# Optimization experiments

Measured on AMD Instinct MI355X. Metric: run time of the kernel, lower is better.

The kernel has to match this reference:

```python
import jax, jax.numpy as jnp
import numpy as np

# Dimensions
B, S, H = 2, 1024, 1024          # batch, seq_len, hidden_size
I, N, R, K = 2048, 16, 64, 4     # mamba: intermediate, state_size, dt_rank, conv_kernel
NH, NKV, HD = 16, 4, 64          # attention heads, kv heads, head_dim
W_ATT, W_SSM = 512, 128          # dual sliding window sizes
IM = 2816                        # SwiGLU intermediate: 256*ceil(1024*4*2/3/256)
EPS = 1e-6
ROPE_THETA = 10000.0
NEG = -1e9


def rms(x, w):
    return x * jax.lax.rsqrt(jnp.mean(x * x, axis=-1, keepdims=True) + EPS) * w


def silu(x):
    return x * jax.nn.sigmoid(x)


def rotary(x):
    # x: [B, S, h, HD]
    pos = jnp.arange(S, dtype=jnp.float32)
    inv = 1.0 / (ROPE_THETA ** (jnp.arange(0, HD, 2, dtype=jnp.float32) / HD))
    f = pos[:, None] * inv                                   # [S, HD/2]
    cos = jnp.concatenate([jnp.cos(f), jnp.cos(f)], -1)[None, :, None, :]
    sin = jnp.concatenate([jnp.sin(f), jnp.sin(f)], -1)[None, :, None, :]
    x1, x2 = x[..., : HD // 2], x[..., HD // 2 :]
    return x * cos + jnp.concatenate([-x2, x1], -1) * sin


def setup_inputs() -> dict:
    key = jax.random.key(0)
    ks = jax.random.split(key, 16)
    g = lambda k, shape, s=0.02: jax.random.normal(k, shape, jnp.float32) * s
    A_log = jnp.log(jnp.arange(1, N + 1, dtype=jnp.float32))[None, :] * jnp.ones((I, 1), jnp.float32)
    return {
        "hidden_states": jax.random.normal(ks[0], (B, S, H), jnp.float32),
        "pre_norm_w": jnp.ones((H,), jnp.float32),
        "in_proj_w": g(ks[1], (2 * I, H)),
        "conv_w": g(ks[2], (I, K), 0.2),
        "conv_b": jnp.zeros((I,), jnp.float32),
        "x_proj_w": g(ks[3], (R + 2 * N, I)),
        "dt_proj_w": g(ks[4], (I, R), 0.1),
        "dt_proj_b": jnp.full((I,), -2.0, jnp.float32),
        "A_log": A_log,
        "D": jnp.ones((I,), jnp.float32),
        "out_proj_w": g(ks[5], (H, I)),
        "ssm_norm_w": jnp.ones((H,), jnp.float32),
        "q_w": g(ks[6], (NH * HD, H)),
        "k_w": g(ks[7], (NKV * HD, H)),
        "v_w": g(ks[8], (NKV * HD, H)),
        "o_w": g(ks[9], (H, NH * HD)),
        "mlp_norm_w": jnp.ones((H,), jnp.float32),
        "gate_w": g(ks[10], (2 * IM, H)),
        "down_w": g(ks[11], (H, IM)),
    }


def reference(hidden_states, pre_norm_w, in_proj_w, conv_w, conv_b, x_proj_w,
              dt_proj_w, dt_proj_b, A_log, D, out_proj_w, ssm_norm_w,
              q_w, k_w, v_w, o_w, mlp_norm_w, gate_w, down_w):
    residual = hidden_states
    hs = rms(hidden_states, pre_norm_w)

    # ---- Mamba mixer (selective scan) ----
    xz = hs @ in_proj_w.T                          # [B,S,2I]
    x, z = jnp.split(xz, 2, -1)
    x_pad = jnp.pad(x, ((0, 0), (K - 1, 0), (0, 0)))  # causal depthwise conv
    xc = sum(conv_w[:, k] * x_pad[:, k : k + S, :] for k in range(K)) + conv_b
    xs = silu(xc)                                  # [B,S,I]
    proj = xs @ x_proj_w.T                         # [B,S,R+2N]
    dt = jax.nn.softplus(proj[..., :R] @ dt_proj_w.T + dt_proj_b)  # [B,S,I]
    Bm, Cm = proj[..., R : R + N], proj[..., R + N :]              # [B,S,N]
    A = -jnp.exp(A_log)                            # [I,N]
    dA = jnp.exp(dt[..., None] * A)                # [B,S,I,N]
    dBx = dt[..., None] * Bm[:, :, None, :] * xs[..., None]        # [B,S,I,N]

    def step(h, t):
        dA_t, dBx_t, C_t = t
        h = h * dA_t + dBx_t                       # [B,I,N]
        return h, jnp.einsum('bin,bn->bi', h, C_t)

    _, ys = jax.lax.scan(step, jnp.zeros((B, I, N), xs.dtype),
                         (dA.swapaxes(0, 1), dBx.swapaxes(0, 1), Cm.swapaxes(0, 1)))
    y = ys.swapaxes(0, 1) + D * xs
    y = y * silu(z)
    ssm_out = y @ out_proj_w.T                     # [B,S,H]

    # ---- fused add-norm ----
    ssm_residual = ssm_out + residual
    ssm_states = rms(ssm_residual, ssm_norm_w)

    # ---- dual sliding-window attention (GQA) ----
    q = rotary((hs @ q_w.T).reshape(B, S, NH, HD))
    k_att = rotary((hs @ k_w.T).reshape(B, S, NKV, HD))
    v_att = (hs @ v_w.T).reshape(B, S, NKV, HD)
    k_ssm = rotary((ssm_states @ k_w.T).reshape(B, S, NKV, HD))
    v_ssm = (ssm_states @ v_w.T).reshape(B, S, NKV, HD)
    rep = NH // NKV
    expand = lambda t: jnp.repeat(t, rep, axis=2)
    scale = HD ** -0.5
    pi = jnp.arange(S)
    d = pi[:, None] - pi[None, :]
    mask_att = (d >= 0) & (d < W_ATT)
    mask_ssm = (d >= 0) & (d < W_SSM)
    s_att = jnp.where(mask_att, jnp.einsum('bqhd,bkhd->bhqk', q, expand(k_att)) * scale, NEG)
    s_ssm = jnp.where(mask_ssm, jnp.einsum('bqhd,bkhd->bhqk', q, expand(k_ssm)) * scale, NEG)
    p = jax.nn.softmax(jnp.concatenate([s_att, s_ssm], -1), axis=-1)  # joint softmax
    p_att, p_ssm = jnp.split(p, 2, -1)
    o = (jnp.einsum('bhqk,bkhd->bqhd', p_att, expand(v_att)) +
         jnp.einsum('bhqk,bkhd->bqhd', p_ssm, expand(v_ssm)))
    att_out = o.reshape(B, S, NH * HD) @ o_w.T

    # ---- fused add-norm + SwiGLU MLP ----
    mlp_residual = att_out + ssm_residual
    x2 = rms(mlp_residual, mlp_norm_w)
    gate, yv = jnp.split(x2 @ gate_w.T, 2, -1)
    out = (silu(gate) * yv) @ down_w.T
    return mlp_residual + out
```

## Files before the change

### kernel.cpp

```cpp
#include <hip/hip_runtime.h>
#include <hip/hip_bf16.h>

using bf16 = __hip_bfloat16;
typedef short sh8 __attribute__((ext_vector_type(8)));
typedef float f32x4 __attribute__((ext_vector_type(4)));

constexpr int B_ = 2, S_ = 1024, H_ = 1024;
constexpr int I_ = 2048, N_ = 16, R_ = 64, K_ = 4;
constexpr int NH_ = 16, NKV_ = 4, HD_ = 64;
constexpr int IM_ = 2816;
constexpr int M_ = B_ * S_;
constexpr float EPS_ = 1e-6f;
constexpr int NC_ = 64;
constexpr int CL_ = S_ / NC_;
constexpr int BI_ = B_ * I_;

__device__ __forceinline__ float bf2f(bf16 v) { return __bfloat162float(v); }
__device__ __forceinline__ unsigned short f2bfu(float f) {
  bf16 h = __float2bfloat16(f);
  return *reinterpret_cast<unsigned short*>(&h);
}

constexpr int WOFF[11] = {
    0,
    4194304,
    4194304 + 196608,
    4390912 + 131072,
    4521984 + 2097152,
    6619136 + 1048576,
    7667712 + 262144,
    7929856 + 262144,
    8192000 + 1048576,
    9240576 + 5767168,
    15007744 + 2883584};
struct WPtrs { const float* p[10]; };

__global__ __launch_bounds__(256) void weights_cvt(WPtrs wp, bf16* __restrict__ dst) {
  int idx4 = blockIdx.x * 256 + threadIdx.x;
  if (idx4 >= WOFF[10] / 4) return;
  int e = idx4 * 4;
  int seg = 0;
#pragma unroll
  for (int s = 1; s < 10; ++s)
    if (e >= WOFF[s]) seg = s;
  float4 v = *(const float4*)(wp.p[seg] + (e - WOFF[seg]));
  ushort4 u = {f2bfu(v.x), f2bfu(v.y), f2bfu(v.z), f2bfu(v.w)};
  *(ushort4*)(dst + e) = u;
}

__global__ __launch_bounds__(256) void rms_kernel(const float* __restrict__ src,
                                                  const float* __restrict__ w,
                                                  bf16* __restrict__ dst, int ncols) {
  int row = blockIdx.x;
  const float* s = src + (size_t)row * ncols;
  float ss = 0.f;
  for (int c = threadIdx.x; c < ncols; c += 256) {
    float v = s[c];
    ss += v * v;
  }
#pragma unroll
  for (int off = 32; off; off >>= 1) ss += __shfl_down(ss, off, 64);
  __shared__ float red[4];
  if ((threadIdx.x & 63) == 0) red[threadIdx.x >> 6] = ss;
  __syncthreads();
  float tot = red[0] + red[1] + red[2] + red[3];
  float sc = rsqrtf(tot / (float)ncols + EPS_);
  for (int c = threadIdx.x; c < ncols; c += 256) {
    dst[(size_t)row * ncols + c] = __float2bfloat16(s[c] * sc * w[c]);
  }
}

__global__ __launch_bounds__(256) void reduce_rms_kernel(const float* __restrict__ parts,
                                                         int np, size_t pstride,
                                                         const float* __restrict__ residual,
                                                         float* __restrict__ sum_out,
                                                         const float* __restrict__ w,
                                                         bf16* __restrict__ dst) {
  int row = blockIdx.x;
  float v[4];
  float ss = 0.f;
#pragma unroll
  for (int e = 0; e < 4; ++e) {
    int c = threadIdx.x + e * 256;
    size_t o = (size_t)row * 1024 + c;
    float s = residual[o];
    for (int p = 0; p < np; ++p) s += parts[(size_t)p * pstride + o];
    v[e] = s;
    sum_out[o] = s;
    ss += s * s;
  }
#pragma unroll
  for (int off = 32; off; off >>= 1) ss += __shfl_down(ss, off, 64);
  __shared__ float red[4];
  if ((threadIdx.x & 63) == 0) red[threadIdx.x >> 6] = ss;
  __syncthreads();
  float tot = red[0] + red[1] + red[2] + red[3];
  float sc = rsqrtf(tot / 1024.f + EPS_);
#pragma unroll
  for (int e = 0; e < 4; ++e) {
    int c = threadIdx.x + e * 256;
    dst[(size_t)row * 1024 + c] = __float2bfloat16(v[e] * sc * w[c]);
  }
}

__global__ __launch_bounds__(256) void reduce_add_kernel(const float* __restrict__ parts,
                                                         int np, size_t pstride,
                                                         const float* __restrict__ residual,
                                                         float* __restrict__ out, int n4) {
  int idx = blockIdx.x * 256 + threadIdx.x;
  if (idx >= n4) return;
  float4 s = ((const float4*)residual)[idx];
  for (int p = 0; p < np; ++p) {
    float4 v = ((const float4*)(parts + (size_t)p * pstride))[idx];
    s.x += v.x; s.y += v.y; s.z += v.z; s.w += v.w;
  }
  ((float4*)out)[idx] = s;
}

__global__ __launch_bounds__(256) void xproj_reduce_kernel(const float* __restrict__ parts,
                                                           int np, size_t pstride,
                                                           float* __restrict__ proj,
                                                           bf16* __restrict__ proj_b, int n4) {
  int idx = blockIdx.x * 256 + threadIdx.x;
  if (idx >= n4) return;
  float4 s = {0.f, 0.f, 0.f, 0.f};
  for (int p = 0; p < np; ++p) {
    float4 v = ((const float4*)(parts + (size_t)p * pstride))[idx];
    s.x += v.x; s.y += v.y; s.z += v.z; s.w += v.w;
  }
  ((float4*)proj)[idx] = s;
  ushort4 u = {f2bfu(s.x), f2bfu(s.y), f2bfu(s.z), f2bfu(s.w)};
  ((ushort4*)proj_b)[idx] = u;
}

template <int MODE>
__global__ __launch_bounds__(256) void mfma_gemm_ep(const bf16* __restrict__ A,
                                                    const bf16* __restrict__ W,
                                                    float* __restrict__ C,
                                                    bf16* __restrict__ Cb,
                                                    int Nn, int Kd, int lda, int kclen,
                                                    size_t pstride,
                                                    const float* __restrict__ biasf) {
  __shared__ bf16 Als[128 * 64];
  __shared__ bf16 Bls[128 * 64];
  const int tid = threadIdx.x;
  const int lane = tid & 63;
  const int wave = tid >> 6;
  const int m0 = blockIdx.y * 128;
  const int n0 = blockIdx.x * 128;
  const int wm = (wave >> 1) * 64;
  const int wn = (wave & 1) * 64;
  const int kbeg = blockIdx.z * kclen;
  const int kend = min(Kd, kbeg + kclen);

  f32x4 acc[4][4] = {};

  for (int k0 = kbeg; k0 < kend; k0 += 64) {
#pragma unroll
    for (int r = 0; r < 4; ++r) {
      int linear = (r * 256 + tid) * 8;
      int row = linear >> 6;
      int col = linear & 63;
      const bf16* gA = A + (size_t)(m0 + row) * lda + (k0 + col);
      __builtin_amdgcn_global_load_lds(
          (const __attribute__((address_space(1))) void*)gA,
          (__attribute__((address_space(3))) void*)&Als[linear], 16, 0, 0);
      int nrow = n0 + row;
      if (nrow < Nn) {
        const bf16* gB = W + (size_t)nrow * Kd + (k0 + col);
        __builtin_amdgcn_global_load_lds(
            (const __attribute__((address_space(1))) void*)gB,
            (__attribute__((address_space(3))) void*)&Bls[linear], 16, 0, 0);
      }
    }
    __syncthreads();
#pragma unroll
    for (int kc = 0; kc < 2; ++kc) {
      const int kb = kc * 32 + (lane >> 4) * 8;
      sh8 af[4], bv[4];
#pragma unroll
      for (int i = 0; i < 4; ++i)
        af[i] = *reinterpret_cast<const sh8*>(&Als[(wm + i * 16 + (lane & 15)) * 64 + kb]);
#pragma unroll
      for (int j = 0; j < 4; ++j)
        bv[j] = *reinterpret_cast<const sh8*>(&Bls[(wn + j * 16 + (lane & 15)) * 64 + kb]);
#pragma unroll
      for (int i = 0; i < 4; ++i)
#pragma unroll
        for (int j = 0; j < 4; ++j)
          acc[i][j] = __builtin_amdgcn_mfma_f32_16x16x32_bf16(af[i], bv[j], acc[i][j], 0, 0, 0);
    }
    __syncthreads();
  }
#pragma unroll
  for (int i = 0; i < 4; ++i) {
#pragma unroll
    for (int j = 0; j < 4; ++j) {
      int col = n0 + wn + j * 16 + (lane & 15);
      if (col < Nn) {
#pragma unroll
        for (int r = 0; r < 4; ++r) {
          int row = m0 + wm + i * 16 + (lane >> 4) * 4 + r;
          size_t o = (size_t)row * Nn + col;
          float v = acc[i][j][r];
          if constexpr (MODE == 5) {
            Cb[o] = __float2bfloat16(v);
          } else if constexpr (MODE == 7) {
            float x = v + biasf[col];
            Cb[o] = __float2bfloat16((x > 20.f) ? x : log1pf(__expf(x)));
          } else if constexpr (MODE == 9) {
            C[(size_t)blockIdx.z * pstride + o] = v;
          }
        }
      }
    }
  }
}

__global__ __launch_bounds__(256) void conv_silu_kernel(const bf16* __restrict__ xz_b,
                                                        const float* __restrict__ cw,
                                                        const float* __restrict__ cb,
                                                        bf16* __restrict__ xs_b,
                                                        bf16* __restrict__ zs_b) {
  int idx4 = blockIdx.x * 256 + threadIdx.x;
  if (idx4 >= M_ * I_ / 4) return;
  int i4 = (idx4 & (I_ / 4 - 1)) * 4;
  int row = idx4 >> 9;
  int t = row & (S_ - 1);
  float4 acc = *(const float4*)(cb + i4);
  float a[4] = {acc.x, acc.y, acc.z, acc.w};
#pragma unroll
  for (int k = 0; k < K_; ++k) {
    int tt = t + k - (K_ - 1);
    if (tt >= 0) {
      const bf16* xp = xz_b + (size_t)(row + k - (K_ - 1)) * (2 * I_) + i4;
#pragma unroll
      for (int e = 0; e < 4; ++e)
        a[e] += cw[(i4 + e) * K_ + k] * bf2f(xp[e]);
    }
  }
  ushort4 xo, zo;
  const bf16* zp = xz_b + (size_t)row * (2 * I_) + I_ + i4;
#pragma unroll
  for (int e = 0; e < 4; ++e) {
    float sg = 1.f / (1.f + __expf(-a[e]));
    ((unsigned short*)&xo)[e] = f2bfu(a[e] * sg);
    float z = bf2f(zp[e]);
    float zg = 1.f / (1.f + __expf(-z));
    ((unsigned short*)&zo)[e] = f2bfu(z * zg);
  }
  *(ushort4*)(xs_b + (size_t)row * I_ + i4) = xo;
  *(ushort4*)(zs_b + (size_t)row * I_ + i4) = zo;
}

__global__ __launch_bounds__(256) void scan1_kernel(const bf16* __restrict__ dt_b,
                                                    const bf16* __restrict__ xs_b,
                                                    const float* __restrict__ proj,
                                                    const float* __restrict__ A_log,
                                                    float* __restrict__ aprod,
                                                    float* __restrict__ hloc) {
  const int b = blockIdx.x >> 3;
  const int i = (blockIdx.x & 7) * 256 + threadIdx.x;
  const int c = blockIdx.y;
  float A[16];
#pragma unroll
  for (int n = 0; n < 16; ++n) A[n] = -__expf(A_log[i * 16 + n]);
  float h[16] = {}, ap[16];
#pragma unroll
  for (int n = 0; n < 16; ++n) ap[n] = 1.f;
  const int t0 = c * CL_;
  for (int t = 0; t < CL_; ++t) {
    int row = b * S_ + t0 + t;
    float d = bf2f(dt_b[(size_t)row * I_ + i]);
    float x = bf2f(xs_b[(size_t)row * I_ + i]);
    const float* prow = proj + (size_t)row * 96 + R_;
    float dx = d * x;
#pragma unroll
    for (int q = 0; q < 4; ++q) {
      float4 Bv = *(const float4*)(prow + q * 4);
      float bvals[4] = {Bv.x, Bv.y, Bv.z, Bv.w};
#pragma unroll
      for (int n = 0; n < 4; ++n) {
        int nn = q * 4 + n;
        float da = __expf(d * A[nn]);
        h[nn] = h[nn] * da + dx * bvals[n];
        ap[nn] *= da;
      }
    }
  }
  size_t o = ((size_t)c * BI_ + (b << 11) + i) * 16;
#pragma unroll
  for (int n = 0; n < 16; ++n) { aprod[o + n] = ap[n]; hloc[o + n] = h[n]; }
}

__global__ __launch_bounds__(256) void scan2_kernel(const float* __restrict__ aprod,
                                                    const float* __restrict__ hloc,
                                                    float* __restrict__ hstart) {
  int j = blockIdx.x * 256 + threadIdx.x;
  float h = 0.f;
  for (int c = 0; c < NC_; ++c) {
    size_t idx = (size_t)c * (BI_ * 16) + j;
    hstart[idx] = h;
    h = aprod[idx] * h + hloc[idx];
  }
}

__global__ __launch_bounds__(256) void scan3_kernel(const bf16* __restrict__ dt_b,
                                                    const bf16* __restrict__ xs_b,
                                                    const float* __restrict__ proj,
                                                    const float* __restrict__ A_log,
                                                    const float* __restrict__ hstart,
                                                    const bf16* __restrict__ zs_b,
                                                    const float* __restrict__ Dp,
                                                    bf16* __restrict__ ys_b) {
  const int b = blockIdx.x >> 3;
  const int i = (blockIdx.x & 7) * 256 + threadIdx.x;
  const int c = blockIdx.y;
  float A[16];
#pragma unroll
  for (int n = 0; n < 16; ++n) A[n] = -__expf(A_log[i * 16 + n]);
  float h[16];
  size_t hs0 = ((size_t)c * BI_ + (b << 11) + i) * 16;
#pragma unroll
  for (int n = 0; n < 16; ++n) h[n] = hstart[hs0 + n];
  float Dv = Dp[i];
  const int t0 = c * CL_;
  for (int t = 0; t < CL_; ++t) {
    int row = b * S_ + t0 + t;
    float d = bf2f(dt_b[(size_t)row * I_ + i]);
    float x = bf2f(xs_b[(size_t)row * I_ + i]);
    const float* prow = proj + (size_t)row * 96 + R_;
    float dx = d * x;
    float y = 0.f;
#pragma unroll
    for (int q = 0; q < 4; ++q) {
      float4 Bv = *(const float4*)(prow + q * 4);
      float4 Cv = *(const float4*)(prow + 16 + q * 4);
      float bvals[4] = {Bv.x, Bv.y, Bv.z, Bv.w};
      float cvals[4] = {Cv.x, Cv.y, Cv.z, Cv.w};
#pragma unroll
      for (int n = 0; n < 4; ++n) {
        int nn = q * 4 + n;
        float da = __expf(d * A[nn]);
        h[nn] = h[nn] * da + dx * bvals[n];
        y += h[nn] * cvals[n];
      }
    }
    float yv = y + Dv * x;
    float zs = bf2f(zs_b[(size_t)row * I_ + i]);
    ys_b[(size_t)row * I_ + i] = __float2bfloat16(yv * zs);
  }
}

__global__ __launch_bounds__(256) void rope_all_kernel(const float* __restrict__ pqkv,
                                                       const float* __restrict__ pkv,
                                                       bf16* __restrict__ qb_b,
                                                       bf16* __restrict__ katt_b,
                                                       bf16* __restrict__ vatt_b,
                                                       bf16* __restrict__ kssm_b,
                                                       bf16* __restrict__ vssm_b) {
  constexpr size_t PQ = (size_t)M_ * 1536;
  constexpr size_t PK = (size_t)M_ * 512;
  int idx = blockIdx.x * 256 + threadIdx.x;
  if (idx >= M_ * 32 * 32) return;
  int j = idx & 31;
  int hs = (idx >> 5) & 31;
  int row = idx >> 10;
  int t = row & (S_ - 1);
  float x1, x2;
  bf16* dst;
  bool rope;
  if (hs < 24) {
    size_t off;
    if (hs < 16) {
      off = (size_t)row * 1536 + hs * 64;
      dst = qb_b + ((size_t)row * 16 + hs) * 64;
      rope = true;
    } else if (hs < 20) {
      off = (size_t)row * 1536 + 1024 + (hs - 16) * 64;
      dst = katt_b + ((size_t)row * 4 + (hs - 16)) * 64;
      rope = true;
    } else {
      off = (size_t)row * 1536 + 1280 + (hs - 20) * 64;
      dst = vatt_b + ((size_t)row * 4 + (hs - 20)) * 64;
      rope = false;
    }
    x1 = pqkv[off + j] + pqkv[PQ + off + j];
    x2 = pqkv[off + 32 + j] + pqkv[PQ + off + 32 + j];
  } else {
    size_t off;
    if (hs < 28) {
      off = (size_t)row * 512 + (hs - 24) * 64;
      dst = kssm_b + ((size_t)row * 4 + (hs - 24)) * 64;
      rope = true;
    } else {
      off = (size_t)row * 512 + 256 + (hs - 28) * 64;
      dst = vssm_b + ((size_t)row * 4 + (hs - 28)) * 64;
      rope = false;
    }
    x1 = 0.f; x2 = 0.f;
#pragma unroll
    for (int p = 0; p < 4; ++p) {
      x1 += pkv[p * PK + off + j];
      x2 += pkv[p * PK + off + 32 + j];
    }
  }
  if (rope) {
    float inv = __expf(-(float)j * (9.210340371976184f / 32.f));
    float f = (float)t * inv;
    float s, c;
    sincosf(f, &s, &c);
    dst[j] = __float2bfloat16(x1 * c - x2 * s);
    dst[32 + j] = __float2bfloat16(x2 * c + x1 * s);
  } else {
    dst[j] = __float2bfloat16(x1);
    dst[32 + j] = __float2bfloat16(x2);
  }
}

__global__ __launch_bounds__(256) void attn_mfma_kernel(const bf16* __restrict__ qb,
                                                        const bf16* __restrict__ katt,
                                                        const bf16* __restrict__ vatt,
                                                        const bf16* __restrict__ kssm,
                                                        const bf16* __restrict__ vssm,
                                                        bf16* __restrict__ ob) {
  constexpr int LDK = 72;
  __shared__ __align__(16) bf16 Qs[64 * LDK];
  __shared__ __align__(16) bf16 Ks[64 * LDK];
  __shared__ __align__(16) bf16 VTs[64 * LDK];
  __shared__ __align__(16) bf16 Ps[4][16 * LDK];

  const int tid = threadIdx.x;
  const int lane = tid & 63;
  const int wave = tid >> 6;
  const int lr = lane & 15;
  const int lg = lane >> 4;
  const int q0 = blockIdx.x * 64;
  const int h = blockIdx.y;
  const int b = blockIdx.z;
  const int kvh = h >> 2;
  const int qw0 = q0 + wave * 16;

#pragma unroll
  for (int i = 0; i < 2; ++i) {
    int g = tid + 256 * i;
    int row = g >> 3, d0 = (g & 7) * 8;
    const bf16* src = qb + ((size_t)((b * S_ + q0 + row) * NH_ + h)) * 64 + d0;
    *(sh8*)&Qs[row * LDK + d0] = *(const sh8*)src;
  }

  f32x4 acc[4] = {};
  float mrow[4], lrow[4];
#pragma unroll
  for (int r = 0; r < 4; ++r) { mrow[r] = -1e30f; lrow[r] = 0.f; }

  __syncthreads();

  for (int it = 0; it < 12; ++it) {
    const bool att = it < 9;
    const int kc = att ? (q0 - 512 + 64 * it) : (q0 - 128 + 64 * (it - 9));
    if (kc + 63 < 0) continue;
    const bf16* kptr = att ? katt : kssm;
    const bf16* vptr = att ? vatt : vssm;
    const int W = att ? 512 : 128;

#pragma unroll
    for (int i = 0; i < 2; ++i) {
      int g = tid + 256 * i;
      int key = g >> 3, d0 = (g & 7) * 8;
      int kp = min(max(kc + key, 0), S_ - 1);
      const bf16* src = kptr + ((size_t)((b * S_ + kp) * NKV_ + kvh)) * 64 + d0;
      *(sh8*)&Ks[key * LDK + d0] = *(const sh8*)src;
    }
#pragma unroll
    for (int i = 0; i < 2; ++i) {
      int g = tid + 256 * i;
      int d = g & 63, kg = (g >> 6) * 8;
      sh8 v;
#pragma unroll
      for (int j = 0; j < 8; ++j) {
        int kp = min(max(kc + kg + j, 0), S_ - 1);
        v[j] = *(const short*)(vptr + ((size_t)((b * S_ + kp) * NKV_ + kvh)) * 64 + d);
      }
      *(sh8*)&VTs[d * LDK + kg] = v;
    }
    __syncthreads();

    bool skip = (kc > qw0 + 15) || (kc + 63 < qw0 - (W - 1));
    if (!skip) {
      float sc[4][4];
#pragma unroll
      for (int t = 0; t < 4; ++t) {
        f32x4 s = {};
#pragma unroll
        for (int kk = 0; kk < 2; ++kk) {
          sh8 a = *(const sh8*)&Qs[(wave * 16 + lr) * LDK + kk * 32 + lg * 8];
          sh8 kf = *(const sh8*)&Ks[(t * 16 + lr) * LDK + kk * 32 + lg * 8];
          s = __builtin_amdgcn_mfma_f32_16x16x32_bf16(a, kf, s, 0, 0, 0);
        }
        int key = kc + t * 16 + lr;
#pragma unroll
        for (int r = 0; r < 4; ++r) {
          int q = qw0 + lg * 4 + r;
          int dq = q - key;
          bool ok = (key >= 0) && (dq >= 0) && (dq < W);
          sc[t][r] = ok ? s[r] * 0.125f : -1e9f;
        }
      }
      float mx[4];
#pragma unroll
      for (int r = 0; r < 4; ++r)
        mx[r] = fmaxf(fmaxf(sc[0][r], sc[1][r]), fmaxf(sc[2][r], sc[3][r]));
#pragma unroll
      for (int off = 1; off < 16; off <<= 1)
#pragma unroll
        for (int r = 0; r < 4; ++r) mx[r] = fmaxf(mx[r], __shfl_xor(mx[r], off));
      float al[4];
#pragma unroll
      for (int r = 0; r < 4; ++r) {
        float mn = fmaxf(mrow[r], mx[r]);
        al[r] = __expf(mrow[r] - mn);
        mrow[r] = mn;
      }
      float rs[4] = {};
#pragma unroll
      for (int t = 0; t < 4; ++t)
#pragma unroll
        for (int r = 0; r < 4; ++r) {
          float p = __expf(sc[t][r] - mrow[r]);
          sc[t][r] = p;
          rs[r] += p;
        }
#pragma unroll
      for (int off = 1; off < 16; off <<= 1)
#pragma unroll
        for (int r = 0; r < 4; ++r) rs[r] += __shfl_xor(rs[r], off);
#pragma unroll
      for (int r = 0; r < 4; ++r) lrow[r] = lrow[r] * al[r] + rs[r];
#pragma unroll
      for (int n = 0; n < 4; ++n)
#pragma unroll
        for (int r = 0; r < 4; ++r) acc[n][r] *= al[r];
#pragma unroll
      for (int t = 0; t < 4; ++t)
#pragma unroll
        for (int r = 0; r < 4; ++r)
          Ps[wave][(lg * 4 + r) * LDK + t * 16 + lr] = __float2bfloat16(sc[t][r]);
#pragma unroll
      for (int n = 0; n < 4; ++n) {
#pragma unroll
        for (int kk = 0; kk < 2; ++kk) {
          sh8 pf = *(const sh8*)&Ps[wave][lr * LDK + kk * 32 + lg * 8];
          sh8 vf = *(const sh8*)&VTs[(n * 16 + lr) * LDK + kk * 32 + lg * 8];
          acc[n] = __builtin_amdgcn_mfma_f32_16x16x32_bf16(pf, vf, acc[n], 0, 0, 0);
        }
      }
    }
    __syncthreads();
  }
#pragma unroll
  for (int n = 0; n < 4; ++n)
#pragma unroll
    for (int r = 0; r < 4; ++r) {
      int q = qw0 + lg * 4 + r;
      int d = n * 16 + lr;
      ob[((size_t)((b * S_ + q) * NH_ + h)) * 64 + d] = __float2bfloat16(acc[n][r] / lrow[r]);
    }
}

__global__ __launch_bounds__(256) void mlp_silu_mul_b(const bf16* __restrict__ gy_b,
                                                      bf16* __restrict__ act_b) {
  int idx4 = blockIdx.x * 256 + threadIdx.x;
  if (idx4 >= M_ * IM_ / 4) return;
  int i4 = (idx4 % (IM_ / 4)) * 4;
  int row = idx4 / (IM_ / 4);
  const bf16* gp = gy_b + (size_t)row * (2 * IM_) + i4;
  const bf16* vp = gy_b + (size_t)row * (2 * IM_) + IM_ + i4;
  ushort4 o;
#pragma unroll
  for (int e = 0; e < 4; ++e) {
    float g = bf2f(gp[e]);
    float v = bf2f(vp[e]);
    float sg = 1.f / (1.f + __expf(-g));
    ((unsigned short*)&o)[e] = f2bfu(g * sg * v);
  }
  *(ushort4*)(act_b + (size_t)row * IM_ + i4) = o;
}

extern "C" void kernel_launch(void* const* d_in, const int* in_sizes, int n_in,
                              void* d_out, int out_size, void* d_ws, size_t ws_size,
                              hipStream_t stream) {
  const float* hidden = (const float*)d_in[0];
  const float* pre_norm_w = (const float*)d_in[1];
  const float* conv_w = (const float*)d_in[3];
  const float* conv_b = (const float*)d_in[4];
  const float* dt_proj_b = (const float*)d_in[7];
  const float* A_log = (const float*)d_in[8];
  const float* Dp = (const float*)d_in[9];
  const float* ssm_norm_w = (const float*)d_in[11];
  const float* mlp_norm_w = (const float*)d_in[16];

  char* base = (char*)d_ws;
  size_t off = 0;
  auto alloc = [&](size_t bytes) {
    size_t p = off;
    off += (bytes + 63) & ~(size_t)63;
    return (void*)(base + p);
  };

  bf16* wb = (bf16*)alloc((size_t)WOFF[10] * 2);
  WPtrs wp;
  wp.p[0] = (const float*)d_in[2];
  wp.p[1] = (const float*)d_in[5];
  wp.p[2] = (const float*)d_in[6];
  wp.p[3] = (const float*)d_in[10];
  wp.p[4] = (const float*)d_in[12];
  wp.p[5] = (const float*)d_in[13];
  wp.p[6] = (const float*)d_in[14];
  wp.p[7] = (const float*)d_in[15];
  wp.p[8] = (const float*)d_in[17];
  wp.p[9] = (const float*)d_in[18];
  const bf16* w_in_proj = wb + WOFF[0];
  const bf16* w_x_proj = wb + WOFF[1];
  const bf16* w_dt_proj = wb + WOFF[2];
  const bf16* w_out_proj = wb + WOFF[3];
  const bf16* w_qkv = wb + WOFF[4];
  const bf16* w_kv = wb + WOFF[5];
  const bf16* w_o = wb + WOFF[7];
  const bf16* w_gate = wb + WOFF[8];
  const bf16* w_down = wb + WOFF[9];

  bf16* xz_b = (bf16*)alloc((size_t)M_ * 2 * IM_ * 2);
  bf16* gy_b = xz_b;
  bf16* xs_b = (bf16*)alloc((size_t)M_ * I_ * 2);
  bf16* zs_b = (bf16*)alloc((size_t)M_ * I_ * 2);
  float* proj = (float*)alloc((size_t)M_ * 96 * 4);
  bf16* proj_b = (bf16*)alloc((size_t)M_ * 96 * 2);
  char* slab = (char*)alloc((size_t)2 * M_ * 1536 * 4);
  bf16* dt_b = (bf16*)slab;
  float* pqkv = (float*)slab;
  float* aprod = (float*)alloc((size_t)BI_ * N_ * NC_ * 4);
  float* pkv = aprod;
  char* redux = (char*)alloc((size_t)2 * BI_ * N_ * NC_ * 4);
  float* hloc = (float*)redux;
  float* hstart = hloc + (size_t)BI_ * N_ * NC_;
  float* px = (float*)redux;
  float* pout = (float*)redux;
  float* ssmres = (float*)alloc((size_t)M_ * H_ * 4);
  float* mlpres = (float*)alloc((size_t)M_ * H_ * 4);
  bf16* hs_b = (bf16*)alloc((size_t)M_ * H_ * 2);
  bf16* x2_b = hs_b;
  bf16* ssmst_b = (bf16*)alloc((size_t)M_ * H_ * 2);
  bf16* scratch_b = (bf16*)alloc((size_t)M_ * IM_ * 2);
  bf16* ys_b = scratch_b;
  bf16* ob_b = scratch_b;
  bf16* act_b = scratch_b;
  bf16* qb_b = (bf16*)alloc((size_t)M_ * NH_ * HD_ * 2);
  bf16* katt_b = (bf16*)alloc((size_t)M_ * NKV_ * HD_ * 2);
  bf16* vatt_b = (bf16*)alloc((size_t)M_ * NKV_ * HD_ * 2);
  bf16* kssm_b = (bf16*)alloc((size_t)M_ * NKV_ * HD_ * 2);
  bf16* vssm_b = (bf16*)alloc((size_t)M_ * NKV_ * HD_ * 2);

  const dim3 blk(256);

  weights_cvt<<<(WOFF[10] / 4 + 255) / 256, 256, 0, stream>>>(wp, wb);
  rms_kernel<<<M_, 256, 0, stream>>>(hidden, pre_norm_w, hs_b, H_);
  mfma_gemm_ep<5><<<dim3(32, 16), blk, 0, stream>>>(hs_b, w_in_proj, nullptr, xz_b,
                                                    2 * I_, H_, H_, H_, 0, nullptr);
  conv_silu_kernel<<<(M_ * I_ / 4 + 255) / 256, 256, 0, stream>>>(xz_b, conv_w, conv_b,
                                                                  xs_b, zs_b);
  mfma_gemm_ep<9><<<dim3(1, 16, 8), blk, 0, stream>>>(xs_b, w_x_proj, px, nullptr,
                                                      96, I_, I_, 256, (size_t)M_ * 96,
                                                      nullptr);
  xproj_reduce_kernel<<<(M_ * 96 / 4 + 255) / 256, 256, 0, stream>>>(px, 8, (size_t)M_ * 96,
                                                                     proj, proj_b,
                                                                     M_ * 96 / 4);
  mfma_gemm_ep<7><<<dim3(16, 16), blk, 0, stream>>>(proj_b, w_dt_proj, nullptr, dt_b,
                                                    I_, R_, 96, R_, 0, dt_proj_b);
  scan1_kernel<<<dim3(16, NC_), 256, 0, stream>>>(dt_b, xs_b, proj, A_log, aprod, hloc);
  scan2_kernel<<<BI_ * N_ / 256, 256, 0, stream>>>(aprod, hloc, hstart);
  scan3_kernel<<<dim3(16, NC_), 256, 0, stream>>>(dt_b, xs_b, proj, A_log, hstart,
                                                  zs_b, Dp, ys_b);
  mfma_gemm_ep<9><<<dim3(8, 16, 4), blk, 0, stream>>>(ys_b, w_out_proj, pout, nullptr,
                                                      H_, I_, I_, 512, (size_t)M_ * H_,
                                                      nullptr);
  reduce_rms_kernel<<<M_, 256, 0, stream>>>(pout, 4, (size_t)M_ * H_, hidden,
                                            ssmres, ssm_norm_w, ssmst_b);
  mfma_gemm_ep<9><<<dim3(12, 16, 2), blk, 0, stream>>>(hs_b, w_qkv, pqkv, nullptr,
                                                       1536, H_, H_, 512,
                                                       (size_t)M_ * 1536, nullptr);
  mfma_gemm_ep<9><<<dim3(4, 16, 4), blk, 0, stream>>>(ssmst_b, w_kv, pkv, nullptr,
                                                      512, H_, H_, 256,
                                                      (size_t)M_ * 512, nullptr);
  rope_all_kernel<<<(M_ * 32 * 32 + 255) / 256, 256, 0, stream>>>(pqkv, pkv, qb_b,
                                                                  katt_b, vatt_b,
                                                                  kssm_b, vssm_b);
  attn_mfma_kernel<<<dim3(S_ / 64, NH_, B_), blk, 0, stream>>>(qb_b, katt_b, vatt_b,
                                                               kssm_b, vssm_b, ob_b);
  mfma_gemm_ep<9><<<dim3(8, 16, 4), blk, 0, stream>>>(ob_b, w_o, pout, nullptr,
                                                      H_, NH_ * HD_, NH_ * HD_, 256,
                                                      (size_t)M_ * H_, nullptr);
  reduce_rms_kernel<<<M_, 256, 0, stream>>>(pout, 4, (size_t)M_ * H_, ssmres,
                                            mlpres, mlp_norm_w, x2_b);
  mfma_gemm_ep<5><<<dim3(44, 16), blk, 0, stream>>>(x2_b, w_gate, nullptr, gy_b,
                                                    2 * IM_, H_, H_, H_, 0, nullptr);
  mlp_silu_mul_b<<<(M_ * IM_ / 4 + 255) / 256, 256, 0, stream>>>(gy_b, act_b);
  mfma_gemm_ep<9><<<dim3(8, 16, 4), blk, 0, stream>>>(act_b, w_down, pout, nullptr,
                                                      H_, IM_, IM_, 704,
                                                      (size_t)M_ * H_, nullptr);
  reduce_add_kernel<<<(M_ * H_ / 4 + 255) / 256, 256, 0, stream>>>(pout, 4, (size_t)M_ * H_,
                                                                   mlpres, (float*)d_out,
                                                                   M_ * H_ / 4);
}
```

Before: 506.1 us.

## Merge in_proj with QKV GEMM and fuse SwiGLU into gate GEMM epilogue

Reorders the packed bf16 weight buffer so in_proj and q/k/v weights are contiguous, letting one GEMM produce both the mamba xz projection (bf16) and the attention qkv (fp32, no split-K). This removes a separate split-K QKV GEMM and its partial-sum reduction in rope. The gate weight rows are interleaved during conversion so gate and up columns sit in adjacent lanes, and a new epilogue computes silu(gate)*up via a lane shuffle, removing the standalone SwiGLU kernel and the gy buffer round-trip. Half the lanes in the new epilogue sit idle at store time, and the merged GEMM grid has no split-K for the qkv part.

```diff
diff --git a/kernel.cpp b/kernel.cpp
--- a/kernel.cpp
+++ b/kernel.cpp
@@ -24,12 +24,12 @@
 constexpr int WOFF[11] = {
     0,
     4194304,
-    4194304 + 196608,
-    4390912 + 131072,
-    4521984 + 2097152,
-    6619136 + 1048576,
-    7667712 + 262144,
-    7929856 + 262144,
+    4194304 + 1048576,
+    5242880 + 262144,
+    5505024 + 262144,
+    5767168 + 196608,
+    5963776 + 131072,
+    6094848 + 2097152,
     8192000 + 1048576,
     9240576 + 5767168,
     15007744 + 2883584};
@@ -43,9 +43,16 @@
 #pragma unroll
   for (int s = 1; s < 10; ++s)
     if (e >= WOFF[s]) seg = s;
-  float4 v = *(const float4*)(wp.p[seg] + (e - WOFF[seg]));
+  int le = e - WOFF[seg];
+  float4 v = *(const float4*)(wp.p[seg] + le);
   ushort4 u = {f2bfu(v.x), f2bfu(v.y), f2bfu(v.z), f2bfu(v.w)};
-  *(ushort4*)(dst + e) = u;
+  int de = le;
+  if (seg == 8) {
+    int row = le >> 10, col = le & 1023;
+    int drow = (row < IM_) ? (2 * row) : (2 * (row - IM_) + 1);
+    de = drow * 1024 + col;
+  }
+  *(ushort4*)(dst + WOFF[seg] + de) = u;
 }
 
 __global__ __launch_bounds__(256) void rms_kernel(const float* __restrict__ src,
@@ -201,15 +208,26 @@
 #pragma unroll
         for (int r = 0; r < 4; ++r) {
           int row = m0 + wm + i * 16 + (lane >> 4) * 4 + r;
-          size_t o = (size_t)row * Nn + col;
           float v = acc[i][j][r];
           if constexpr (MODE == 5) {
-            Cb[o] = __float2bfloat16(v);
+            Cb[(size_t)row * Nn + col] = __float2bfloat16(v);
           } else if constexpr (MODE == 7) {
             float x = v + biasf[col];
-            Cb[o] = __float2bfloat16((x > 20.f) ? x : log1pf(__expf(x)));
+            Cb[(size_t)row * Nn + col] =
+                __float2bfloat16((x > 20.f) ? x : log1pf(__expf(x)));
           } else if constexpr (MODE == 9) {
-            C[(size_t)blockIdx.z * pstride + o] = v;
+            C[(size_t)blockIdx.z * pstride + (size_t)row * Nn + col] = v;
+          } else if constexpr (MODE == 10) {
+            if (col < 4096)
+              Cb[(size_t)row * 4096 + col] = __float2bfloat16(v);
+            else
+              C[(size_t)row * 1536 + (col - 4096)] = v;
+          } else if constexpr (MODE == 11) {
+            float ov = __shfl_xor(v, 1);
+            if ((lane & 1) == 0) {
+              float sg = 1.f / (1.f + __expf(-v));
+              Cb[(size_t)row * IM_ + (col >> 1)] = __float2bfloat16(v * sg * ov);
+            }
           }
         }
       }
@@ -352,14 +370,13 @@
   }
 }
 
-__global__ __launch_bounds__(256) void rope_all_kernel(const float* __restrict__ pqkv,
+__global__ __launch_bounds__(256) void rope_all_kernel(const float* __restrict__ qkv,
                                                        const float* __restrict__ pkv,
                                                        bf16* __restrict__ qb_b,
                                                        bf16* __restrict__ katt_b,
                                                        bf16* __restrict__ vatt_b,
                                                        bf16* __restrict__ kssm_b,
                                                        bf16* __restrict__ vssm_b) {
-  constexpr size_t PQ = (size_t)M_ * 1536;
   constexpr size_t PK = (size_t)M_ * 512;
   int idx = blockIdx.x * 256 + threadIdx.x;
   if (idx >= M_ * 32 * 32) return;
@@ -385,8 +402,8 @@
       dst = vatt_b + ((size_t)row * 4 + (hs - 20)) * 64;
       rope = false;
     }
-    x1 = pqkv[off + j] + pqkv[PQ + off + j];
-    x2 = pqkv[off + 32 + j] + pqkv[PQ + off + 32 + j];
+    x1 = qkv[off + j];
+    x2 = qkv[off + 32 + j];
   } else {
     size_t off;
     if (hs < 28) {
@@ -566,25 +583,6 @@
       int d = n * 16 + lr;
       ob[((size_t)((b * S_ + q) * NH_ + h)) * 64 + d] = __float2bfloat16(acc[n][r] / lrow[r]);
     }
-}
-
-__global__ __launch_bounds__(256) void mlp_silu_mul_b(const bf16* __restrict__ gy_b,
-                                                      bf16* __restrict__ act_b) {
-  int idx4 = blockIdx.x * 256 + threadIdx.x;
-  if (idx4 >= M_ * IM_ / 4) return;
-  int i4 = (idx4 % (IM_ / 4)) * 4;
-  int row = idx4 / (IM_ / 4);
-  const bf16* gp = gy_b + (size_t)row * (2 * IM_) + i4;
-  const bf16* vp = gy_b + (size_t)row * (2 * IM_) + IM_ + i4;
-  ushort4 o;
-#pragma unroll
-  for (int e = 0; e < 4; ++e) {
-    float g = bf2f(gp[e]);
-    float v = bf2f(vp[e]);
-    float sg = 1.f / (1.f + __expf(-g));
-    ((unsigned short*)&o)[e] = f2bfu(g * sg * v);
-  }
-  *(ushort4*)(act_b + (size_t)row * IM_ + i4) = o;
 }
 
 extern "C" void kernel_launch(void* const* d_in, const int* in_sizes, int n_in,
@@ -611,34 +609,31 @@
   bf16* wb = (bf16*)alloc((size_t)WOFF[10] * 2);
   WPtrs wp;
   wp.p[0] = (const float*)d_in[2];
-  wp.p[1] = (const float*)d_in[5];
-  wp.p[2] = (const float*)d_in[6];
-  wp.p[3] = (const float*)d_in[10];
-  wp.p[4] = (const float*)d_in[12];
-  wp.p[5] = (const float*)d_in[13];
-  wp.p[6] = (const float*)d_in[14];
+  wp.p[1] = (const float*)d_in[12];
+  wp.p[2] = (const float*)d_in[13];
+  wp.p[3] = (const float*)d_in[14];
+  wp.p[4] = (const float*)d_in[5];
+  wp.p[5] = (const float*)d_in[6];
+  wp.p[6] = (const float*)d_in[10];
   wp.p[7] = (const float*)d_in[15];
   wp.p[8] = (const float*)d_in[17];
   wp.p[9] = (const float*)d_in[18];
-  const bf16* w_in_proj = wb + WOFF[0];
-  const bf16* w_x_proj = wb + WOFF[1];
-  const bf16* w_dt_proj = wb + WOFF[2];
-  const bf16* w_out_proj = wb + WOFF[3];
-  const bf16* w_qkv = wb + WOFF[4];
-  const bf16* w_kv = wb + WOFF[5];
+  const bf16* w_inqkv = wb + WOFF[0];
+  const bf16* w_kv = wb + WOFF[2];
+  const bf16* w_x_proj = wb + WOFF[4];
+  const bf16* w_dt_proj = wb + WOFF[5];
+  const bf16* w_out_proj = wb + WOFF[6];
   const bf16* w_o = wb + WOFF[7];
   const bf16* w_gate = wb + WOFF[8];
   const bf16* w_down = wb + WOFF[9];
 
-  bf16* xz_b = (bf16*)alloc((size_t)M_ * 2 * IM_ * 2);
-  bf16* gy_b = xz_b;
+  bf16* xz_b = (bf16*)alloc((size_t)M_ * 2 * I_ * 2);
   bf16* xs_b = (bf16*)alloc((size_t)M_ * I_ * 2);
   bf16* zs_b = (bf16*)alloc((size_t)M_ * I_ * 2);
   float* proj = (float*)alloc((size_t)M_ * 96 * 4);
   bf16* proj_b = (bf16*)alloc((size_t)M_ * 96 * 2);
-  char* slab = (char*)alloc((size_t)2 * M_ * 1536 * 4);
-  bf16* dt_b = (bf16*)slab;
-  float* pqkv = (float*)slab;
+  float* qkv = (float*)alloc((size_t)M_ * 1536 * 4);
+  bf16* dt_b = (bf16*)alloc((size_t)M_ * I_ * 2);
   float* aprod = (float*)alloc((size_t)BI_ * N_ * NC_ * 4);
   float* pkv = aprod;
   char* redux = (char*)alloc((size_t)2 * BI_ * N_ * NC_ * 4);
@@ -650,11 +645,11 @@
   float* mlpres = (float*)alloc((size_t)M_ * H_ * 4);
   bf16* hs_b = (bf16*)alloc((size_t)M_ * H_ * 2);
   bf16* x2_b = hs_b;
-  bf16* ssmst_b = (bf16*)alloc((size_t)M_ * H_ * 2);
   bf16* scratch_b = (bf16*)alloc((size_t)M_ * IM_ * 2);
   bf16* ys_b = scratch_b;
   bf16* ob_b = scratch_b;
   bf16* act_b = scratch_b;
+  bf16* ssmst_b = (bf16*)alloc((size_t)M_ * H_ * 2);
   bf16* qb_b = (bf16*)alloc((size_t)M_ * NH_ * HD_ * 2);
   bf16* katt_b = (bf16*)alloc((size_t)M_ * NKV_ * HD_ * 2);
   bf16* vatt_b = (bf16*)alloc((size_t)M_ * NKV_ * HD_ * 2);
@@ -665,8 +660,8 @@
 
   weights_cvt<<<(WOFF[10] / 4 + 255) / 256, 256, 0, stream>>>(wp, wb);
   rms_kernel<<<M_, 256, 0, stream>>>(hidden, pre_norm_w, hs_b, H_);
-  mfma_gemm_ep<5><<<dim3(32, 16), blk, 0, stream>>>(hs_b, w_in_proj, nullptr, xz_b,
-                                                    2 * I_, H_, H_, H_, 0, nullptr);
+  mfma_gemm_ep<10><<<dim3(44, 16), blk, 0, stream>>>(hs_b, w_inqkv, qkv, xz_b,
+                                                     5632, H_, H_, H_, 0, nullptr);
   conv_silu_kernel<<<(M_ * I_ / 4 + 255) / 256, 256, 0, stream>>>(xz_b, conv_w, conv_b,
                                                                   xs_b, zs_b);
   mfma_gemm_ep<9><<<dim3(1, 16, 8), blk, 0, stream>>>(xs_b, w_x_proj, px, nullptr,
@@ -686,13 +681,10 @@
                                                       nullptr);
   reduce_rms_kernel<<<M_, 256, 0, stream>>>(pout, 4, (size_t)M_ * H_, hidden,
                                             ssmres, ssm_norm_w, ssmst_b);
-  mfma_gemm_ep<9><<<dim3(12, 16, 2), blk, 0, stream>>>(hs_b, w_qkv, pqkv, nullptr,
-                                                       1536, H_, H_, 512,
-                                                       (size_t)M_ * 1536, nullptr);
   mfma_gemm_ep<9><<<dim3(4, 16, 4), blk, 0, stream>>>(ssmst_b, w_kv, pkv, nullptr,
                                                       512, H_, H_, 256,
                                                       (size_t)M_ * 512, nullptr);
-  rope_all_kernel<<<(M_ * 32 * 32 + 255) / 256, 256, 0, stream>>>(pqkv, pkv, qb_b,
+  rope_all_kernel<<<(M_ * 32 * 32 + 255) / 256, 256, 0, stream>>>(qkv, pkv, qb_b,
                                                                   katt_b, vatt_b,
                                                                   kssm_b, vssm_b);
   attn_mfma_kernel<<<dim3(S_ / 64, NH_, B_), blk, 0, stream>>>(qb_b, katt_b, vatt_b,
@@ -702,9 +694,8 @@
                                                       (size_t)M_ * H_, nullptr);
   reduce_rms_kernel<<<M_, 256, 0, stream>>>(pout, 4, (size_t)M_ * H_, ssmres,
                                             mlpres, mlp_norm_w, x2_b);
-  mfma_gemm_ep<5><<<dim3(44, 16), blk, 0, stream>>>(x2_b, w_gate, nullptr, gy_b,
-                                                    2 * IM_, H_, H_, H_, 0, nullptr);
-  mlp_silu_mul_b<<<(M_ * IM_ / 4 + 255) / 256, 256, 0, stream>>>(gy_b, act_b);
+  mfma_gemm_ep<11><<<dim3(44, 16), blk, 0, stream>>>(x2_b, w_gate, nullptr, act_b,
+                                                     2 * IM_, H_, H_, H_, 0, nullptr);
   mfma_gemm_ep<9><<<dim3(8, 16, 4), blk, 0, stream>>>(act_b, w_down, pout, nullptr,
                                                       H_, IM_, IM_, 704,
                                                       (size_t)M_ * H_, nullptr);
```

After: 493.1 us. 1.03x faster.
